# Performance work log

Hardware: AMD Instinct MI355X
Metric: run time of the kernel (lower is better)

## Reference

```python
import jax, jax.numpy as jnp
import numpy as np

DIM, DK, DV = 1024, 128, 128

def setup_inputs() -> dict:
    key = jax.random.key(0)
    ks = jax.random.split(key, 7)
    X = jax.random.normal(ks[0], (4, 4096, DIM), dtype=jnp.float32)
    s = DIM ** -0.5
    Wq = jax.random.normal(ks[1], (DIM, DK), dtype=jnp.float32) * s
    bq = jnp.zeros((DK,), dtype=jnp.float32)
    Wk = jax.random.normal(ks[2], (DIM, DK), dtype=jnp.float32) * s
    bk = jnp.zeros((DK,), dtype=jnp.float32)
    Wv = jax.random.normal(ks[3], (DIM, DV), dtype=jnp.float32) * s
    bv = jnp.zeros((DV,), dtype=jnp.float32)
    return {"X": X, "Wq": Wq, "bq": bq, "Wk": Wk, "bk": bk, "Wv": Wv, "bv": bv}

def reference(X, Wq, bq, Wk, bk, Wv, bv):
    scale = DK ** -0.5
    q = X @ Wq + bq              # [B, S, dk]
    k = X @ Wk + bk              # [B, S, dk]
    v = X @ Wv + bv              # [B, S, dv]
    attn = jnp.einsum('bqd,bkd->bqk', q, k) * scale  # [B, S, S]
    attn = jax.nn.softmax(attn, axis=-1)
    return jnp.einsum('bqk,bkd->bqd', attn, v)       # [B, S, dv]
```

## Files before the change

kernel.cpp:

```cpp
#include <hip/hip_runtime.h>

#define NB 4
#define SEQ 4096
#define DIMK 1024
#define DKV 128
#define SCALE 0.08838834764831845f

typedef float  f32x4  __attribute__((ext_vector_type(4)));
typedef float  f32x16 __attribute__((ext_vector_type(16)));
typedef _Float16 f16x8 __attribute__((ext_vector_type(8)));

static __device__ __forceinline__ int pkrtz(float a, float b) {
    auto h = __builtin_amdgcn_cvt_pkrtz(a, b);
    return __builtin_bit_cast(int, h);
}

__global__ void prep_wt(const float* __restrict__ Wq, const float* __restrict__ Wk,
                        const float* __restrict__ Wv, _Float16* __restrict__ WT) {
    int tid = blockIdx.x * 256 + threadIdx.x;
    int n  = tid & 127;
    int k  = (tid >> 7) & 1023;
    int w3 = tid >> 17;
    const float* W = (w3 == 0) ? Wq : (w3 == 1) ? Wk : Wv;
    WT[((size_t)w3 * 128 + n) * 1024 + k] = (_Float16)W[(size_t)k * 128 + n];
}

__global__ __launch_bounds__(256) void qkv_proj(
    const float* __restrict__ X,
    const float* __restrict__ bq, const float* __restrict__ bk, const float* __restrict__ bv,
    const _Float16* __restrict__ WT,
    _Float16* __restrict__ Qh, _Float16* __restrict__ Kh, _Float16* __restrict__ VTh) {

    __shared__ __attribute__((aligned(16))) _Float16 WTs[128 * 40];
    const int t = threadIdx.x;
    const int w = t >> 6, l = t & 63;
    const int lrow = l & 15, lg = l >> 4;
    const int w3   = blockIdx.x % 3;
    const int tile = blockIdx.x / 3;
    const int r0 = tile * 64;

    f32x4 acc[8] = {};
    const float* xrow = X + (size_t)(r0 + w * 16 + lrow) * DIMK;
    const _Float16* Wbase = WT + (size_t)w3 * 128 * 1024;

    float4 xc0 = *(const float4*)(xrow + lg * 8);
    float4 xc1 = *(const float4*)(xrow + lg * 8 + 4);

    for (int k0 = 0; k0 < DIMK; k0 += 32) {
        __syncthreads();
        #pragma unroll
        for (int i = 0; i < 2; ++i) {
            int c = t + 256 * i;
            int row = c >> 2, part = c & 3;
            *(int4*)((char*)WTs + row * 80 + part * 16) =
                *(const int4*)(Wbase + (size_t)row * 1024 + k0 + part * 8);
        }
        float4 xn0, xn1;
        if (k0 + 32 < DIMK) {
            xn0 = *(const float4*)(xrow + k0 + 32 + lg * 8);
            xn1 = *(const float4*)(xrow + k0 + 32 + lg * 8 + 4);
        }
        __syncthreads();
        f16x8 a;
        a[0] = (_Float16)xc0.x; a[1] = (_Float16)xc0.y; a[2] = (_Float16)xc0.z; a[3] = (_Float16)xc0.w;
        a[4] = (_Float16)xc1.x; a[5] = (_Float16)xc1.y; a[6] = (_Float16)xc1.z; a[7] = (_Float16)xc1.w;

        #pragma unroll
        for (int n = 0; n < 8; ++n) {
            f16x8 bf = *(const f16x8*)((const char*)WTs + (n * 16 + lrow) * 80 + lg * 16);
            acc[n] = __builtin_amdgcn_mfma_f32_16x16x32_f16(a, bf, acc[n], 0, 0, 0);
        }
        xc0 = xn0; xc1 = xn1;
    }
    const float* bias = (w3 == 0) ? bq : (w3 == 1) ? bk : bv;
    #pragma unroll
    for (int n = 0; n < 8; ++n) {
        int col = n * 16 + lrow;
        float bv_ = bias[col];
        #pragma unroll
        for (int j = 0; j < 4; ++j) {
            int grow = r0 + w * 16 + lg * 4 + j;
            float val = acc[n][j] + bv_;
            if (w3 == 0) {
                Qh[(size_t)grow * DKV + col] = (_Float16)(val * SCALE);
            } else if (w3 == 1) {
                Kh[(size_t)grow * DKV + col] = (_Float16)val;
            } else {
                int b = grow >> 12, sp = grow & 4095;
                VTh[((size_t)b * DKV + col) * SEQ + sp] = (_Float16)val;
            }
        }
    }
}

__global__ __launch_bounds__(256, 2) void attn_kernel(
    const _Float16* __restrict__ Qh, const _Float16* __restrict__ Kh,
    const _Float16* __restrict__ VTh, float* __restrict__ out) {

    __shared__ __attribute__((aligned(16))) char lds[65536];

    const int t = threadIdx.x;
    const int w = t >> 6, l = t & 63;
    const int lq = l & 31;
    const int hi = l >> 5;

    const int work = (blockIdx.x & 7) * 64 + (blockIdx.x >> 3);
    const int b  = work >> 7;
    const int qt = work & 127;
    const int q0 = qt * 32;

    char* Kw = lds + w * 16384;
    char* Vw = Kw + 8192;

    f16x8 qf[8];
    #pragma unroll
    for (int c = 0; c < 8; ++c)
        qf[c] = *(const f16x8*)(Qh + (size_t)(b * SEQ + q0 + lq) * DKV + c * 16 + hi * 8);

    f32x16 o[4] = {};
    float m = -INFINITY, lsum = 0.f;

    for (int kt = 0; kt < 32; ++kt) {
        const int k0 = w * 1024 + kt * 32;

        #pragma unroll
        for (int i = 0; i < 8; ++i) {
            int c = l + 64 * i; int row = c >> 4, part = c & 15;
            *(int4*)(Kw + row * 256 + ((part * 16) ^ ((row & 7) << 4))) =
                *(const int4*)(Kh + (size_t)(b * SEQ + k0 + row) * DKV + part * 8);
        }
        #pragma unroll
        for (int i = 0; i < 8; ++i) {
            int c = l + 64 * i; int dv = c >> 2, p = c & 3;
            *(int4*)(Vw + dv * 64 + ((p ^ ((dv >> 1) & 3)) * 16)) =
                *(const int4*)(VTh + (size_t)(b * DKV + dv) * SEQ + k0 + p * 8);
        }
        asm volatile("s_waitcnt lgkmcnt(0)" ::: "memory");
        __builtin_amdgcn_sched_barrier(0);

        f32x16 s = {};
        #pragma unroll
        for (int c = 0; c < 8; ++c) {
            f16x8 kf = *(const f16x8*)(Kw + lq * 256 +
                                       (((2 * c + hi) * 16) ^ ((lq & 7) << 4)));
            s = __builtin_amdgcn_mfma_f32_32x32x16_f16(kf, qf[c], s, 0, 0, 0);
        }

        float tm = -INFINITY;
        #pragma unroll
        for (int r = 0; r < 16; ++r) tm = fmaxf(tm, s[r]);
        tm = fmaxf(tm, __shfl_xor(tm, 32));

        if (__any(tm > m + 8.f)) {
            float mnew = fmaxf(m, tm);
            float corr = __expf(m - mnew);
            m = mnew;
            lsum *= corr;
            #pragma unroll
            for (int dvt = 0; dvt < 4; ++dvt) o[dvt] *= corr;
        }
        float ts = 0.f;
        #pragma unroll
        for (int r = 0; r < 16; ++r) { s[r] = __expf(s[r] - m); ts += s[r]; }
        ts += __shfl_xor(ts, 32);
        lsum += ts;

        int wv[8];
        #pragma unroll
        for (int i = 0; i < 8; ++i) wv[i] = pkrtz(s[2 * i], s[2 * i + 1]);

        #pragma unroll
        for (int s_ = 0; s_ < 2; ++s_) {
            const int base = s_ * 4;
            int x0 = __shfl_xor(wv[base + 0], 32);
            int x1 = __shfl_xor(wv[base + 1], 32);
            int x2 = __shfl_xor(wv[base + 2], 32);
            int x3 = __shfl_xor(wv[base + 3], 32);
            union { int i[4]; f16x8 v; } bu;
            bu.i[0] = hi ? x2 : wv[base + 0];
            bu.i[1] = hi ? x3 : wv[base + 1];
            bu.i[2] = hi ? wv[base + 2] : x0;
            bu.i[3] = hi ? wv[base + 3] : x1;
            #pragma unroll
            for (int dvt = 0; dvt < 4; ++dvt) {
                int row = dvt * 32 + lq;
                f16x8 vf = *(const f16x8*)(Vw + row * 64 +
                                           (((s_ * 2 + hi) ^ ((row >> 1) & 3)) * 16));
                o[dvt] = __builtin_amdgcn_mfma_f32_32x32x16_f16(vf, bu.v, o[dvt], 0, 0, 0);
            }
        }
    }

    float* obuf  = (float*)lds;
    float* mlbuf = (float*)(lds + 49152);

    __syncthreads();
    if (w == 1 || w == 3) {
        int sb = (w == 3);
        #pragma unroll
        for (int dvt = 0; dvt < 4; ++dvt)
            #pragma unroll
            for (int r = 0; r < 16; ++r)
                obuf[sb * 4096 + (dvt * 16 + r) * 64 + l] = o[dvt][r];
        if (l < 32) {
            mlbuf[sb * 64 + l * 2 + 0] = m;
            mlbuf[sb * 64 + l * 2 + 1] = lsum;
        }
    }
    __syncthreads();
    if (w == 0 || w == 2) {
        int sb = (w == 2);
        float mo  = mlbuf[sb * 64 + lq * 2 + 0];
        float lo_ = mlbuf[sb * 64 + lq * 2 + 1];
        float mn = fmaxf(m, mo);
        float ca = __expf(m - mn);
        float cb = __expf(mo - mn);
        m = mn;
        lsum = lsum * ca + lo_ * cb;
        #pragma unroll
        for (int dvt = 0; dvt < 4; ++dvt)
            #pragma unroll
            for (int r = 0; r < 16; ++r)
                o[dvt][r] = o[dvt][r] * ca + obuf[sb * 4096 + (dvt * 16 + r) * 64 + l] * cb;
    }
    __syncthreads();
    if (w == 2) {
        #pragma unroll
        for (int dvt = 0; dvt < 4; ++dvt)
            #pragma unroll
            for (int r = 0; r < 16; ++r)
                obuf[(dvt * 16 + r) * 64 + l] = o[dvt][r];
        if (l < 32) {
            mlbuf[l * 2 + 0] = m;
            mlbuf[l * 2 + 1] = lsum;
        }
    }
    __syncthreads();
    if (w == 0) {
        float mo  = mlbuf[lq * 2 + 0];
        float lo_ = mlbuf[lq * 2 + 1];
        float mn = fmaxf(m, mo);
        float ca = __expf(m - mn);
        float cb = __expf(mo - mn);
        float rl = 1.0f / (lsum * ca + lo_ * cb);
        #pragma unroll
        for (int dvt = 0; dvt < 4; ++dvt)
            #pragma unroll
            for (int r = 0; r < 16; ++r)
                o[dvt][r] = (o[dvt][r] * ca + obuf[(dvt * 16 + r) * 64 + l] * cb) * rl;
    }
    __syncthreads();
    float* tbuf = (float*)lds;
    if (w == 0) {
        #pragma unroll
        for (int dvt = 0; dvt < 4; ++dvt)
            #pragma unroll
            for (int r = 0; r < 16; ++r) {
                int dv = dvt * 32 + (r & 3) + 8 * (r >> 2) + 4 * hi;
                tbuf[lq * 132 + dv] = o[dvt][r];
            }
    }
    __syncthreads();
    const size_t obase = (size_t)(b * SEQ + qt * 32) * DKV;
    int row = t >> 3, c0 = (t & 7) * 16;
    #pragma unroll
    for (int i = 0; i < 4; ++i) {
        float4 v = *(const float4*)(tbuf + row * 132 + c0 + i * 4);
        *(float4*)(out + obase + row * 128 + c0 + i * 4) = v;
    }
}

extern "C" void kernel_launch(void* const* d_in, const int* in_sizes, int n_in,
                              void* d_out, int out_size, void* d_ws, size_t ws_size,
                              hipStream_t stream) {
    const float* X  = (const float*)d_in[0];
    const float* Wq = (const float*)d_in[1];
    const float* bq = (const float*)d_in[2];
    const float* Wk = (const float*)d_in[3];
    const float* bk = (const float*)d_in[4];
    const float* Wv = (const float*)d_in[5];
    const float* bv = (const float*)d_in[6];
    float* out = (float*)d_out;

    const size_t nqe = (size_t)NB * SEQ * DKV;
    _Float16* Qh  = (_Float16*)d_ws;
    _Float16* Kh  = Qh  + nqe;
    _Float16* VTh = Kh  + nqe;
    _Float16* WTh = VTh + nqe;

    prep_wt<<<(3 * 1024 * 128) / 256, 256, 0, stream>>>(Wq, Wk, Wv, WTh);
    qkv_proj<<<(NB * SEQ / 64) * 3, 256, 0, stream>>>(X, bq, bk, bv, WTh, Qh, Kh, VTh);
    attn_kernel<<<NB * 128, 256, 0, stream>>>(Qh, Kh, VTh, out);
}
```

Before: 124.8 us.

## Load MFMA operands directly from global memory, dropping LDS staging

Both the QKV projection and the attention kernel now read their MFMA B/K/V fragments straight from global memory (relying on L1/L2 caching) instead of staging tiles through shared memory. This removes the LDS write/read round trips and the block barriers in the projection loop, and cuts attention LDS to only the final reduction buffers. The smaller LDS footprint lets the occupancy hint rise from 2 to 3 blocks per CU. The risk is higher global load latency, with less explicit reuse exposed on the MFMA critical path.

```diff
diff --git a/kernel.cpp b/kernel.cpp
--- a/kernel.cpp
+++ b/kernel.cpp
@@ -31,7 +31,6 @@
     const _Float16* __restrict__ WT,
     _Float16* __restrict__ Qh, _Float16* __restrict__ Kh, _Float16* __restrict__ VTh) {
 
-    __shared__ __attribute__((aligned(16))) _Float16 WTs[128 * 40];
     const int t = threadIdx.x;
     const int w = t >> 6, l = t & 63;
     const int lrow = l & 15, lg = l >> 4;
@@ -41,33 +40,24 @@
 
     f32x4 acc[8] = {};
     const float* xrow = X + (size_t)(r0 + w * 16 + lrow) * DIMK;
-    const _Float16* Wbase = WT + (size_t)w3 * 128 * 1024;
+    const _Float16* Wb = WT + ((size_t)w3 * 128 + lrow) * 1024 + lg * 8;
 
     float4 xc0 = *(const float4*)(xrow + lg * 8);
     float4 xc1 = *(const float4*)(xrow + lg * 8 + 4);
 
     for (int k0 = 0; k0 < DIMK; k0 += 32) {
-        __syncthreads();
-        #pragma unroll
-        for (int i = 0; i < 2; ++i) {
-            int c = t + 256 * i;
-            int row = c >> 2, part = c & 3;
-            *(int4*)((char*)WTs + row * 80 + part * 16) =
-                *(const int4*)(Wbase + (size_t)row * 1024 + k0 + part * 8);
-        }
         float4 xn0, xn1;
         if (k0 + 32 < DIMK) {
             xn0 = *(const float4*)(xrow + k0 + 32 + lg * 8);
             xn1 = *(const float4*)(xrow + k0 + 32 + lg * 8 + 4);
         }
-        __syncthreads();
         f16x8 a;
         a[0] = (_Float16)xc0.x; a[1] = (_Float16)xc0.y; a[2] = (_Float16)xc0.z; a[3] = (_Float16)xc0.w;
         a[4] = (_Float16)xc1.x; a[5] = (_Float16)xc1.y; a[6] = (_Float16)xc1.z; a[7] = (_Float16)xc1.w;
 
         #pragma unroll
         for (int n = 0; n < 8; ++n) {
-            f16x8 bf = *(const f16x8*)((const char*)WTs + (n * 16 + lrow) * 80 + lg * 16);
+            f16x8 bf = *(const f16x8*)(Wb + (size_t)n * 16 * 1024 + k0);
             acc[n] = __builtin_amdgcn_mfma_f32_16x16x32_f16(a, bf, acc[n], 0, 0, 0);
         }
         xc0 = xn0; xc1 = xn1;
@@ -93,11 +83,11 @@
     }
 }
 
-__global__ __launch_bounds__(256, 2) void attn_kernel(
+__global__ __launch_bounds__(256, 3) void attn_kernel(
     const _Float16* __restrict__ Qh, const _Float16* __restrict__ Kh,
     const _Float16* __restrict__ VTh, float* __restrict__ out) {
 
-    __shared__ __attribute__((aligned(16))) char lds[65536];
+    __shared__ __attribute__((aligned(16))) char lds[33536];
 
     const int t = threadIdx.x;
     const int w = t >> 6, l = t & 63;
@@ -109,9 +99,6 @@
     const int qt = work & 127;
     const int q0 = qt * 32;
 
-    char* Kw = lds + w * 16384;
-    char* Vw = Kw + 8192;
-
     f16x8 qf[8];
     #pragma unroll
     for (int c = 0; c < 8; ++c)
@@ -120,29 +107,14 @@
     f32x16 o[4] = {};
     float m = -INFINITY, lsum = 0.f;
 
+    const _Float16* Kp = Kh + (size_t)(b * SEQ + w * 1024 + lq) * DKV + hi * 8;
+    const _Float16* Vp = VTh + ((size_t)b * DKV + lq) * SEQ + w * 1024 + hi * 8;
+
     for (int kt = 0; kt < 32; ++kt) {
-        const int k0 = w * 1024 + kt * 32;
-
-        #pragma unroll
-        for (int i = 0; i < 8; ++i) {
-            int c = l + 64 * i; int row = c >> 4, part = c & 15;
-            *(int4*)(Kw + row * 256 + ((part * 16) ^ ((row & 7) << 4))) =
-                *(const int4*)(Kh + (size_t)(b * SEQ + k0 + row) * DKV + part * 8);
-        }
-        #pragma unroll
-        for (int i = 0; i < 8; ++i) {
-            int c = l + 64 * i; int dv = c >> 2, p = c & 3;
-            *(int4*)(Vw + dv * 64 + ((p ^ ((dv >> 1) & 3)) * 16)) =
-                *(const int4*)(VTh + (size_t)(b * DKV + dv) * SEQ + k0 + p * 8);
-        }
-        asm volatile("s_waitcnt lgkmcnt(0)" ::: "memory");
-        __builtin_amdgcn_sched_barrier(0);
-
         f32x16 s = {};
         #pragma unroll
         for (int c = 0; c < 8; ++c) {
-            f16x8 kf = *(const f16x8*)(Kw + lq * 256 +
-                                       (((2 * c + hi) * 16) ^ ((lq & 7) << 4)));
+            f16x8 kf = *(const f16x8*)(Kp + c * 16);
             s = __builtin_amdgcn_mfma_f32_32x32x16_f16(kf, qf[c], s, 0, 0, 0);
         }
 
@@ -183,16 +155,16 @@
             bu.i[3] = hi ? wv[base + 3] : x1;
             #pragma unroll
             for (int dvt = 0; dvt < 4; ++dvt) {
-                int row = dvt * 32 + lq;
-                f16x8 vf = *(const f16x8*)(Vw + row * 64 +
-                                           (((s_ * 2 + hi) ^ ((row >> 1) & 3)) * 16));
+                f16x8 vf = *(const f16x8*)(Vp + (size_t)dvt * 32 * SEQ + s_ * 16);
                 o[dvt] = __builtin_amdgcn_mfma_f32_32x32x16_f16(vf, bu.v, o[dvt], 0, 0, 0);
             }
         }
+        Kp += 32 * DKV;
+        Vp += 32;
     }
 
     float* obuf  = (float*)lds;
-    float* mlbuf = (float*)(lds + 49152);
+    float* mlbuf = (float*)(lds + 32768);
 
     __syncthreads();
     if (w == 1 || w == 3) {
```

Result: slower. 242.8 us (+94.5%).

## Double-buffer K tiles in LDS, load V directly to registers, use exp2

Applied to the files above, without the earlier changes.

The attention loop now prefetches the next K tile into registers while the current tile is being computed, and writes it into an alternate LDS buffer after the PV MMAs. This removes the per-iteration wait on LDS stores. V fragments are loaded straight from global memory into registers, so they no longer pass through LDS. Q is prescaled by log2(e)/sqrt(dk) so that exp2f can replace __expf. The swizzle is widened to 16 rows. Register pressure rises from holding the kreg and vreg arrays, and there is no barrier between the LDS write and the next read, which relies on each wave owning its own buffer.

```diff
diff --git a/kernel.cpp b/kernel.cpp
--- a/kernel.cpp
+++ b/kernel.cpp
@@ -5,6 +5,7 @@
 #define DIMK 1024
 #define DKV 128
 #define SCALE 0.08838834764831845f
+#define QSCALE 0.1275174272f
 
 typedef float  f32x4  __attribute__((ext_vector_type(4)));
 typedef float  f32x16 __attribute__((ext_vector_type(16)));
@@ -82,7 +83,7 @@
             int grow = r0 + w * 16 + lg * 4 + j;
             float val = acc[n][j] + bv_;
             if (w3 == 0) {
-                Qh[(size_t)grow * DKV + col] = (_Float16)(val * SCALE);
+                Qh[(size_t)grow * DKV + col] = (_Float16)(val * QSCALE);
             } else if (w3 == 1) {
                 Kh[(size_t)grow * DKV + col] = (_Float16)val;
             } else {
@@ -109,8 +110,8 @@
     const int qt = work & 127;
     const int q0 = qt * 32;
 
-    char* Kw = lds + w * 16384;
-    char* Vw = Kw + 8192;
+    char* bufA = lds + w * 16384;
+    char* bufB = bufA + 8192;
 
     f16x8 qf[8];
     #pragma unroll
@@ -120,76 +121,100 @@
     f32x16 o[4] = {};
     float m = -INFINITY, lsum = 0.f;
 
-    for (int kt = 0; kt < 32; ++kt) {
-        const int k0 = w * 1024 + kt * 32;
-
+    const _Float16* Kbase = Kh + (size_t)(b * SEQ + w * 1024) * DKV;
+    const _Float16* Vbase = VTh + ((size_t)b * DKV + lq) * SEQ + w * 1024 + hi * 8;
+
+    {
+        int4 kreg[8];
         #pragma unroll
         for (int i = 0; i < 8; ++i) {
             int c = l + 64 * i; int row = c >> 4, part = c & 15;
-            *(int4*)(Kw + row * 256 + ((part * 16) ^ ((row & 7) << 4))) =
-                *(const int4*)(Kh + (size_t)(b * SEQ + k0 + row) * DKV + part * 8);
+            kreg[i] = *(const int4*)(Kbase + (size_t)row * DKV + part * 8);
         }
         #pragma unroll
         for (int i = 0; i < 8; ++i) {
-            int c = l + 64 * i; int dv = c >> 2, p = c & 3;
-            *(int4*)(Vw + dv * 64 + ((p ^ ((dv >> 1) & 3)) * 16)) =
-                *(const int4*)(VTh + (size_t)(b * DKV + dv) * SEQ + k0 + p * 8);
-        }
-        asm volatile("s_waitcnt lgkmcnt(0)" ::: "memory");
-        __builtin_amdgcn_sched_barrier(0);
-
-        f32x16 s = {};
-        #pragma unroll
-        for (int c = 0; c < 8; ++c) {
-            f16x8 kf = *(const f16x8*)(Kw + lq * 256 +
-                                       (((2 * c + hi) * 16) ^ ((lq & 7) << 4)));
-            s = __builtin_amdgcn_mfma_f32_32x32x16_f16(kf, qf[c], s, 0, 0, 0);
-        }
-
-        float tm = -INFINITY;
-        #pragma unroll
-        for (int r = 0; r < 16; ++r) tm = fmaxf(tm, s[r]);
-        tm = fmaxf(tm, __shfl_xor(tm, 32));
-
-        if (__any(tm > m + 8.f)) {
-            float mnew = fmaxf(m, tm);
-            float corr = __expf(m - mnew);
-            m = mnew;
-            lsum *= corr;
-            #pragma unroll
-            for (int dvt = 0; dvt < 4; ++dvt) o[dvt] *= corr;
-        }
-        float ts = 0.f;
-        #pragma unroll
-        for (int r = 0; r < 16; ++r) { s[r] = __expf(s[r] - m); ts += s[r]; }
-        ts += __shfl_xor(ts, 32);
-        lsum += ts;
-
-        int wv[8];
-        #pragma unroll
-        for (int i = 0; i < 8; ++i) wv[i] = pkrtz(s[2 * i], s[2 * i + 1]);
-
-        #pragma unroll
-        for (int s_ = 0; s_ < 2; ++s_) {
-            const int base = s_ * 4;
-            int x0 = __shfl_xor(wv[base + 0], 32);
-            int x1 = __shfl_xor(wv[base + 1], 32);
-            int x2 = __shfl_xor(wv[base + 2], 32);
-            int x3 = __shfl_xor(wv[base + 3], 32);
-            union { int i[4]; f16x8 v; } bu;
-            bu.i[0] = hi ? x2 : wv[base + 0];
-            bu.i[1] = hi ? x3 : wv[base + 1];
-            bu.i[2] = hi ? wv[base + 2] : x0;
-            bu.i[3] = hi ? wv[base + 3] : x1;
-            #pragma unroll
-            for (int dvt = 0; dvt < 4; ++dvt) {
-                int row = dvt * 32 + lq;
-                f16x8 vf = *(const f16x8*)(Vw + row * 64 +
-                                           (((s_ * 2 + hi) ^ ((row >> 1) & 3)) * 16));
-                o[dvt] = __builtin_amdgcn_mfma_f32_32x32x16_f16(vf, bu.v, o[dvt], 0, 0, 0);
-            }
-        }
-    }
+            int c = l + 64 * i; int row = c >> 4, part = c & 15;
+            *(int4*)(bufA + row * 256 + ((part * 16) ^ ((row & 15) << 4))) = kreg[i];
+        }
+    }
+
+#define BODY(RD, WR, KT) {                                                                 \
+                         \
+        f16x8 vreg[8];                                                                     \
+        _Pragma("unroll")                                                                  \
+        for (int i = 0; i < 8; ++i) {                                                      \
+            int dvt = i >> 1, s_ = i & 1;                                                  \
+            vreg[i] = *(const f16x8*)(Vbase + (size_t)(dvt * 32) * SEQ +                   \
+                                      (KT) * 32 + s_ * 16);                                \
+        }                                                                                  \
+               \
+        const int ktn = ((KT) + 1) & 31;                                                   \
+        int4 kreg[8];                                                                      \
+        _Pragma("unroll")                                                                  \
+        for (int i = 0; i < 8; ++i) {                                                      \
+            int c = l + 64 * i; int row = c >> 4, part = c & 15;                           \
+            kreg[i] = *(const int4*)(Kbase + (size_t)(ktn * 32 + row) * DKV + part * 8);   \
+        }                                                                                  \
+                                                          \
+        f32x16 s = {};                                                                     \
+        _Pragma("unroll")                                                                  \
+        for (int c = 0; c < 8; ++c) {                                                      \
+            f16x8 kf = *(const f16x8*)((RD) + lq * 256 +                                   \
+                                       (((2 * c + hi) * 16) ^ ((lq & 15) << 4)));          \
+            s = __builtin_amdgcn_mfma_f32_32x32x16_f16(kf, qf[c], s, 0, 0, 0);             \
+        }                                                                                  \
+                                             \
+        float tm = -INFINITY;                                                              \
+        _Pragma("unroll")                                                                  \
+        for (int r = 0; r < 16; ++r) tm = fmaxf(tm, s[r]);                                 \
+        tm = fmaxf(tm, __shfl_xor(tm, 32));                                                \
+        if (__any(tm > m + 8.f)) {                                                         \
+            float mnew = fmaxf(m, tm);                                                     \
+            float corr = exp2f(m - mnew);                                                  \
+            m = mnew; lsum *= corr;                                                        \
+            o[0] *= corr; o[1] *= corr; o[2] *= corr; o[3] *= corr;                        \
+        }                                                                                  \
+        float ts = 0.f;                                                                    \
+        _Pragma("unroll")                                                                  \
+        for (int r = 0; r < 16; ++r) { s[r] = exp2f(s[r] - m); ts += s[r]; }               \
+        ts += __shfl_xor(ts, 32);                                                          \
+        lsum += ts;                                                                        \
+                                                                        \
+        int wv[8];                                                                         \
+        _Pragma("unroll")                                                                  \
+        for (int i = 0; i < 8; ++i) wv[i] = pkrtz(s[2 * i], s[2 * i + 1]);                 \
+                                                 \
+        _Pragma("unroll")                                                                  \
+        for (int s_ = 0; s_ < 2; ++s_) {                                                   \
+            const int base = s_ * 4;                                                       \
+            int x0 = __shfl_xor(wv[base + 0], 32);                                         \
+            int x1 = __shfl_xor(wv[base + 1], 32);                                         \
+            int x2 = __shfl_xor(wv[base + 2], 32);                                         \
+            int x3 = __shfl_xor(wv[base + 3], 32);                                         \
+            union { int i[4]; f16x8 v; } bu;                                               \
+            bu.i[0] = hi ? x2 : wv[base + 0];                                              \
+            bu.i[1] = hi ? x3 : wv[base + 1];                                              \
+            bu.i[2] = hi ? wv[base + 2] : x0;                                              \
+            bu.i[3] = hi ? wv[base + 3] : x1;                                              \
+            _Pragma("unroll")                                                              \
+            for (int dvt = 0; dvt < 4; ++dvt)                                              \
+                o[dvt] = __builtin_amdgcn_mfma_f32_32x32x16_f16(vreg[dvt * 2 + s_], bu.v,  \
+                                                                o[dvt], 0, 0, 0);          \
+        }                                                                                  \
+                                                   \
+        _Pragma("unroll")                                                                  \
+        for (int i = 0; i < 8; ++i) {                                                      \
+            int c = l + 64 * i; int row = c >> 4, part = c & 15;                           \
+            *(int4*)((WR) + row * 256 + ((part * 16) ^ ((row & 15) << 4))) = kreg[i];      \
+        }                                                                                  \
+    }
+
+    #pragma unroll 1
+    for (int kt2 = 0; kt2 < 16; ++kt2) {
+        BODY(bufA, bufB, kt2 * 2)
+        BODY(bufB, bufA, kt2 * 2 + 1)
+    }
+#undef BODY
 
     float* obuf  = (float*)lds;
     float* mlbuf = (float*)(lds + 49152);
@@ -213,8 +238,8 @@
         float mo  = mlbuf[sb * 64 + lq * 2 + 0];
         float lo_ = mlbuf[sb * 64 + lq * 2 + 1];
         float mn = fmaxf(m, mo);
-        float ca = __expf(m - mn);
-        float cb = __expf(mo - mn);
+        float ca = exp2f(m - mn);
+        float cb = exp2f(mo - mn);
         m = mn;
         lsum = lsum * ca + lo_ * cb;
         #pragma unroll
@@ -240,8 +265,8 @@
         float mo  = mlbuf[lq * 2 + 0];
         float lo_ = mlbuf[lq * 2 + 1];
         float mn = fmaxf(m, mo);
-        float ca = __expf(m - mn);
-        float cb = __expf(mo - mn);
+        float ca = exp2f(m - mn);
+        float cb = exp2f(mo - mn);
         float rl = 1.0f / (lsum * ca + lo_ * cb);
         #pragma unroll
         for (int dvt = 0; dvt < 4; ++dvt)
```

After: 138.0 us. +10.6%, slower.

## Prefetch next K/V tile into registers while computing current tile

Applied to the files above, without the earlier changes.

Restructures the per-wave attention loop so the next K and V tiles are loaded from global memory into registers before the QK and PV MFMAs of the current tile, then written to LDS after compute. This aims to hide global load latency behind matrix work. It also widens the K LDS XOR swizzle from 8 to 16 rows to reduce bank conflicts. The cost is 16 extra int4 registers per lane, which may lower occupancy, plus a wasted wrap-around load on the last iteration.

```diff
diff --git a/kernel.cpp b/kernel.cpp
--- a/kernel.cpp
+++ b/kernel.cpp
@@ -120,21 +120,42 @@
     f32x16 o[4] = {};
     float m = -INFINITY, lsum = 0.f;
 
+    const _Float16* Kbase = Kh + (size_t)(b * SEQ + w * 1024) * DKV;
+    const _Float16* Vbase = VTh + (size_t)b * DKV * SEQ + w * 1024;
+
+    const int krow = l >> 4, kpart = l & 15;
+    const int vdv  = l >> 2, vp = l & 3;
+
+    {
+        int4 kreg[8], vreg[8];
+        #pragma unroll
+        for (int i = 0; i < 8; ++i)
+            kreg[i] = *(const int4*)(Kbase + (size_t)(krow + 4 * i) * DKV + kpart * 8);
+        #pragma unroll
+        for (int i = 0; i < 8; ++i)
+            vreg[i] = *(const int4*)(Vbase + (size_t)(vdv + 16 * i) * SEQ + vp * 8);
+        #pragma unroll
+        for (int i = 0; i < 8; ++i) {
+            int row = krow + 4 * i;
+            *(int4*)(Kw + row * 256 + ((kpart * 16) ^ ((row & 15) << 4))) = kreg[i];
+        }
+        #pragma unroll
+        for (int i = 0; i < 8; ++i) {
+            int dv = vdv + 16 * i;
+            *(int4*)(Vw + dv * 64 + ((vp ^ ((dv >> 1) & 3)) * 16)) = vreg[i];
+        }
+    }
+
     for (int kt = 0; kt < 32; ++kt) {
-        const int k0 = w * 1024 + kt * 32;
-
-        #pragma unroll
-        for (int i = 0; i < 8; ++i) {
-            int c = l + 64 * i; int row = c >> 4, part = c & 15;
-            *(int4*)(Kw + row * 256 + ((part * 16) ^ ((row & 7) << 4))) =
-                *(const int4*)(Kh + (size_t)(b * SEQ + k0 + row) * DKV + part * 8);
-        }
-        #pragma unroll
-        for (int i = 0; i < 8; ++i) {
-            int c = l + 64 * i; int dv = c >> 2, p = c & 3;
-            *(int4*)(Vw + dv * 64 + ((p ^ ((dv >> 1) & 3)) * 16)) =
-                *(const int4*)(VTh + (size_t)(b * DKV + dv) * SEQ + k0 + p * 8);
-        }
+        const int kn = ((kt + 1) & 31) * 32;
+        int4 kreg[8], vreg[8];
+        #pragma unroll
+        for (int i = 0; i < 8; ++i)
+            kreg[i] = *(const int4*)(Kbase + (size_t)(kn + krow + 4 * i) * DKV + kpart * 8);
+        #pragma unroll
+        for (int i = 0; i < 8; ++i)
+            vreg[i] = *(const int4*)(Vbase + (size_t)(vdv + 16 * i) * SEQ + kn + vp * 8);
+
         asm volatile("s_waitcnt lgkmcnt(0)" ::: "memory");
         __builtin_amdgcn_sched_barrier(0);
 
@@ -142,7 +163,7 @@
         #pragma unroll
         for (int c = 0; c < 8; ++c) {
             f16x8 kf = *(const f16x8*)(Kw + lq * 256 +
-                                       (((2 * c + hi) * 16) ^ ((lq & 7) << 4)));
+                                       (((2 * c + hi) * 16) ^ ((lq & 15) << 4)));
             s = __builtin_amdgcn_mfma_f32_32x32x16_f16(kf, qf[c], s, 0, 0, 0);
         }
 
@@ -183,11 +204,22 @@
             bu.i[3] = hi ? wv[base + 3] : x1;
             #pragma unroll
             for (int dvt = 0; dvt < 4; ++dvt) {
-                int row = dvt * 32 + lq;
-                f16x8 vf = *(const f16x8*)(Vw + row * 64 +
-                                           (((s_ * 2 + hi) ^ ((row >> 1) & 3)) * 16));
+                int rv = dvt * 32 + lq;
+                f16x8 vf = *(const f16x8*)(Vw + rv * 64 +
+                                           (((s_ * 2 + hi) ^ ((rv >> 1) & 3)) * 16));
                 o[dvt] = __builtin_amdgcn_mfma_f32_32x32x16_f16(vf, bu.v, o[dvt], 0, 0, 0);
             }
+        }
+
+        #pragma unroll
+        for (int i = 0; i < 8; ++i) {
+            int row = krow + 4 * i;
+            *(int4*)(Kw + row * 256 + ((kpart * 16) ^ ((row & 15) << 4))) = kreg[i];
+        }
+        #pragma unroll
+        for (int i = 0; i < 8; ++i) {
+            int dv = vdv + 16 * i;
+            *(int4*)(Vw + dv * 64 + ((vp ^ ((dv >> 1) & 3)) * 16)) = vreg[i];
         }
     }
 
```

After: 124.6 us. No clear change (-0.2%).
